# Kernel tuning notes

Hardware: AMD Instinct MI355X
Metric: run time of the kernel (lower is better)

## Reference

```python
import jax, jax.numpy as jnp
import numpy as np

B, T, C, H = 16, 2048, 1024, 128  # BATCH_SIZE, BLOCK_SIZE, EMBEDDING_SIZE, HEAD_SIZE


def setup_inputs() -> dict:
    key = jax.random.key(0)
    kx, kk, kq, kv = jax.random.split(key, 4)
    x = jax.random.normal(kx, (B, T, C), dtype=jnp.float32)
    # torch Linear(C, H, bias=False): y = x @ W^T with W [H, C]; we store W^T as [C, H]
    scale = C ** -0.5
    Wk = jax.random.normal(kk, (C, H), dtype=jnp.float32) * scale
    Wq = jax.random.normal(kq, (C, H), dtype=jnp.float32) * scale
    Wv = jax.random.normal(kv, (C, H), dtype=jnp.float32) * scale
    return {"x": x, "Wk": Wk, "Wq": Wq, "Wv": Wv}


def reference(x, Wk, Wq, Wv):
    # projections: [B, T, H]
    k = jnp.einsum("btc,ch->bth", x, Wk)
    q = jnp.einsum("btc,ch->bth", x, Wq)
    v = jnp.einsum("btc,ch->bth", x, Wv)
    # scaled scores: [B, T, T]
    scores = jnp.einsum("bqh,bkh->bqk", q, k) * (H ** -0.5)
    # causal mask (tril) then softmax over keys
    causal = jnp.tril(jnp.ones((T, T), dtype=bool))
    scores = jnp.where(causal, scores, -jnp.inf)
    weights = jax.nn.softmax(scores, axis=-1)
    # dropout with p=0.0 is identity (eval mode)
    return jnp.einsum("bqk,bkh->bqh", weights, v)
```

## Files before the change

### kernel.cpp

```cpp
#include <hip/hip_runtime.h>
#include <cmath>

#define B_ 16
#define T_ 2048
#define C_ 1024
#define H_ 128

#define BQ 64
#define BK 64
#define PS 68

#define PM 64
#define PK 64

typedef __bf16 bf16;
typedef bf16 bf16x8 __attribute__((ext_vector_type(8)));
typedef bf16 bf16x4 __attribute__((ext_vector_type(4)));
typedef float f32x4 __attribute__((ext_vector_type(4)));

#define GL_LDS16(gptr, lptr)                                                     \
    __builtin_amdgcn_global_load_lds(                                            \
        (const __attribute__((address_space(1))) unsigned int*)(gptr),           \
        (__attribute__((address_space(3))) unsigned int*)(lptr), 16, 0, 0)

__global__ __launch_bounds__(256) void convert_w(
    const float* __restrict__ Wq, const float* __restrict__ Wk,
    const float* __restrict__ Wv, bf16* __restrict__ wt)
{
    int gid = blockIdx.x * 256 + threadIdx.x;
    int w   = gid >> 14;
    int rem = gid & 16383;
    int n   = rem >> 7;
    int k0  = (rem & 127) * 8;
    const float* src = (w == 0) ? Wq : (w == 1) ? Wk : Wv;
    bf16x8 o;
#pragma unroll
    for (int j = 0; j < 8; ++j) o[j] = (bf16)src[(size_t)(k0 + j) * H_ + n];
    *(bf16x8*)(wt + (size_t)w * (H_ * C_) + (size_t)n * C_ + k0) = o;
}

__global__ __launch_bounds__(256, 2) void proj_mfma(
    const float* __restrict__ x, const bf16* __restrict__ wt,
    bf16* __restrict__ qb, bf16* __restrict__ kb, bf16* __restrict__ vtp)
{
    __shared__ bf16 xs[PM * PK];
    __shared__ bf16 ws[3 * H_ * PK];

    const int tid  = threadIdx.x;
    const int wave = tid >> 6;
    const int lane = tid & 63;
    const int quad = lane >> 4;
    const int lq   = lane & 15;
    const int wr   = wave >> 1;
    const int wc   = wave & 1;
    const int m0   = blockIdx.x * PM;

    f32x4 acc[3][2][4];
#pragma unroll
    for (int w = 0; w < 3; ++w)
#pragma unroll
        for (int mt = 0; mt < 2; ++mt)
#pragma unroll
            for (int nt = 0; nt < 4; ++nt)
                acc[w][mt][nt] = (f32x4){0.f, 0.f, 0.f, 0.f};

    int woff[12];
#pragma unroll
    for (int j = 0; j < 12; ++j) {
        int s  = (wave * 12 + j) * 64 + lane;
        int w  = s >> 10;
        int n  = (s >> 3) & 127;
        int cs = s & 7;
        int c  = cs ^ (n & 7);
        woff[j] = w * (H_ * C_) + n * C_ + c * 8;
    }
    int xoff[4], xslot[4];
#pragma unroll
    for (int j = 0; j < 4; ++j) {
        int f4  = j * 256 + tid;
        int row = f4 >> 4;
        int c4  = f4 & 15;
        int c   = c4 >> 1, half = c4 & 1;
        xoff[j]  = (m0 + row) * C_ + c4 * 4;
        xslot[j] = (row * 8 + (c ^ (row & 7))) * 8 + half * 4;
    }

    for (int k0 = 0; k0 < C_; k0 += PK) {
        __syncthreads();
#pragma unroll
        for (int j = 0; j < 12; ++j) {
            GL_LDS16(wt + woff[j] + k0, (char*)ws + (wave * 12 + j) * 1024);
        }
#pragma unroll
        for (int j = 0; j < 4; ++j) {
            float4 v = *(const float4*)(x + (size_t)xoff[j] + k0);
            bf16x4 o = {(bf16)v.x, (bf16)v.y, (bf16)v.z, (bf16)v.w};
            *(bf16x4*)&xs[xslot[j]] = o;
        }
        __syncthreads();

#pragma unroll
        for (int kc = 0; kc < 2; ++kc) {
            const int c = kc * 4 + quad;
            bf16x8 af[2];
#pragma unroll
            for (int mt = 0; mt < 2; ++mt) {
                int row  = wr * 32 + mt * 16 + lq;
                int slot = row * 8 + (c ^ (row & 7));
                af[mt] = *(const bf16x8*)&xs[slot * 8];
            }
#pragma unroll
            for (int w = 0; w < 3; ++w) {
#pragma unroll
                for (int nt = 0; nt < 4; ++nt) {
                    int n    = wc * 64 + nt * 16 + lq;
                    int slot = n * 8 + (c ^ (n & 7));
                    bf16x8 bfr = *(const bf16x8*)&ws[w * (H_ * PK) + slot * 8];
                    acc[w][0][nt] = __builtin_amdgcn_mfma_f32_16x16x32_bf16(af[0], bfr, acc[w][0][nt], 0, 0, 0);
                    acc[w][1][nt] = __builtin_amdgcn_mfma_f32_16x16x32_bf16(af[1], bfr, acc[w][1][nt], 0, 0, 0);
                }
            }
        }
    }

    const int b  = m0 >> 11;
    const int t0 = m0 & (T_ - 1);
#pragma unroll
    for (int w = 0; w < 2; ++w) {
        bf16* dst = (w == 0) ? qb : kb;
#pragma unroll
        for (int mt = 0; mt < 2; ++mt)
#pragma unroll
            for (int nt = 0; nt < 4; ++nt)
#pragma unroll
                for (int r = 0; r < 4; ++r) {
                    int row = m0 + wr * 32 + mt * 16 + quad * 4 + r;
                    int h   = wc * 64 + nt * 16 + lq;
                    dst[(size_t)row * H_ + h] = (bf16)acc[w][mt][nt][r];
                }
    }
#pragma unroll
    for (int mt = 0; mt < 2; ++mt)
#pragma unroll
        for (int nt = 0; nt < 4; ++nt) {
            int h = wc * 64 + nt * 16 + lq;
            int t = t0 + wr * 32 + mt * 16 + quad * 4;
            bf16x4 o = {(bf16)acc[2][mt][nt][0], (bf16)acc[2][mt][nt][1],
                        (bf16)acc[2][mt][nt][2], (bf16)acc[2][mt][nt][3]};
            *(bf16x4*)&vtp[((size_t)b * H_ + h) * T_ + t] = o;
        }
}

__global__ __launch_bounds__(256) void attn_mfma(
    const bf16* __restrict__ qb, const bf16* __restrict__ kb,
    const bf16* __restrict__ vt, float* __restrict__ out)
{
    __shared__ bf16 Ks[2][BK * 128];
    __shared__ bf16 Vs[2][128 * BK];
    __shared__ bf16 Ps[4][16 * PS];

    const int tid  = threadIdx.x;
    const int wave = tid >> 6;
    const int lane = tid & 63;
    const int quad = lane >> 4;
    const int lq   = lane & 15;

    const int bid = blockIdx.x;
    const int b   = bid & 15;
    const int jq  = bid >> 4;
    const int t0b = (31 - jq) * BQ;
    const int qt0 = t0b + wave * 16;

    const bf16* qrow = qb + ((size_t)b * T_ + qt0 + lq) * H_ + quad * 8;
    bf16x8 qf[4];
#pragma unroll
    for (int c = 0; c < 4; ++c) qf[c] = *(const bf16x8*)(qrow + 32 * c);

    f32x4 acc[8];
#pragma unroll
    for (int i = 0; i < 8; ++i) acc[i] = (f32x4){0.f, 0.f, 0.f, 0.f};
    f32x4 l_acc = (f32x4){0.f, 0.f, 0.f, 0.f};

    bf16x8 ones;
#pragma unroll
    for (int j = 0; j < 8; ++j) ones[j] = (bf16)1.0f;

    const float SC2 = 0.12751749985029928f;
    const int ntiles = t0b / BK + 1;

    const bf16* Kg = kb + (size_t)b * T_ * H_;
    const bf16* Vg = vt + (size_t)b * H_ * T_;
    bf16* Pw = &Ps[wave][0];

    int koff[4], voff[4], dst8[4];
#pragma unroll
    for (int j = 0; j < 4; ++j) {
        int p   = (j * 4 + wave) * 64 + lane;
        int r   = p >> 4, pos = p & 15;
        int l   = (pos & 8) | ((pos & 7) ^ (r & 7));
        koff[j] = r * H_ + l * 8;
        int hh  = p >> 3, pos2 = p & 7;
        voff[j] = hh * T_ + (pos2 ^ (hh & 7)) * 8;
        dst8[j] = (j * 4 + wave) * 64 * 8;
    }
    int swk[4], swv[2];
#pragma unroll
    for (int c = 0; c < 4; ++c) {
        int l = quad + 4 * c;
        swk[c] = (l & 8) | ((l & 7) ^ (lq & 7));
    }
#pragma unroll
    for (int kc = 0; kc < 2; ++kc) swv[kc] = (quad + 4 * kc) ^ (lq & 7);

#pragma unroll
    for (int j = 0; j < 4; ++j) {
        GL_LDS16(Kg + (size_t)koff[j], &Ks[0][dst8[j]]);
        GL_LDS16(Vg + (size_t)voff[j], &Vs[0][dst8[j]]);
    }

    for (int kt = 0; kt < ntiles; ++kt) {
        __syncthreads();
        if (kt + 1 < ntiles) {
            const int k1 = (kt + 1) * BK;
            const int nb = (kt + 1) & 1;
#pragma unroll
            for (int j = 0; j < 4; ++j) {
                GL_LDS16(Kg + (size_t)k1 * H_ + koff[j], &Ks[nb][dst8[j]]);
                GL_LDS16(Vg + (size_t)(k1 + voff[j]),    &Vs[nb][dst8[j]]);
            }
        }
        const bf16* Kb = &Ks[kt & 1][0];
        const bf16* Vb = &Vs[kt & 1][0];
        const bool finalt = (kt == ntiles - 1);

#pragma unroll
        for (int ns = 0; ns < 4; ++ns) {
            if (!finalt || ns <= wave) {
                f32x4 sv = (f32x4){0.f, 0.f, 0.f, 0.f};
#pragma unroll
                for (int c = 0; c < 4; ++c) {
                    bf16x8 kf = *(const bf16x8*)&Kb[((ns * 16 + lq) * 16 + swk[c]) * 8];
                    sv = __builtin_amdgcn_mfma_f32_16x16x32_bf16(qf[c], kf, sv, 0, 0, 0);
                }
                if (finalt && ns == wave) {
#pragma unroll
                    for (int r = 0; r < 4; ++r) {
                        float p = (lq <= quad * 4 + r) ? exp2f(sv[r] * SC2) : 0.f;
                        Pw[(quad * 4 + r) * PS + ns * 16 + lq] = (bf16)p;
                    }
                } else {
#pragma unroll
                    for (int r = 0; r < 4; ++r) {
                        Pw[(quad * 4 + r) * PS + ns * 16 + lq] = (bf16)exp2f(sv[r] * SC2);
                    }
                }
            } else {
#pragma unroll
                for (int r = 0; r < 4; ++r)
                    Pw[(quad * 4 + r) * PS + ns * 16 + lq] = (bf16)0.f;
            }
        }

        bf16x8 pf[2];
#pragma unroll
        for (int kc = 0; kc < 2; ++kc)
            pf[kc] = *(const bf16x8*)&Pw[lq * PS + kc * 32 + quad * 8];

        l_acc = __builtin_amdgcn_mfma_f32_16x16x32_bf16(pf[0], ones, l_acc, 0, 0, 0);
        l_acc = __builtin_amdgcn_mfma_f32_16x16x32_bf16(pf[1], ones, l_acc, 0, 0, 0);

#pragma unroll
        for (int ht = 0; ht < 8; ++ht) {
#pragma unroll
            for (int kc = 0; kc < 2; ++kc) {
                bf16x8 vf = *(const bf16x8*)&Vb[((ht * 16 + lq) * 8 + swv[kc]) * 8];
                acc[ht] = __builtin_amdgcn_mfma_f32_16x16x32_bf16(pf[kc], vf, acc[ht], 0, 0, 0);
            }
        }
    }

    float inv[4];
#pragma unroll
    for (int r = 0; r < 4; ++r) inv[r] = 1.f / l_acc[r];
#pragma unroll
    for (int ht = 0; ht < 8; ++ht) {
#pragma unroll
        for (int r = 0; r < 4; ++r) {
            out[((size_t)b * T_ + qt0 + quad * 4 + r) * H_ + ht * 16 + lq] = acc[ht][r] * inv[r];
        }
    }
}

extern "C" void kernel_launch(void* const* d_in, const int* in_sizes, int n_in,
                              void* d_out, int out_size, void* d_ws, size_t ws_size,
                              hipStream_t stream) {
    const float* x  = (const float*)d_in[0];
    const float* Wk = (const float*)d_in[1];
    const float* Wq = (const float*)d_in[2];
    const float* Wv = (const float*)d_in[3];
    float* out = (float*)d_out;

    bf16* qb = (bf16*)d_ws;
    bf16* kb = qb + (size_t)B_ * T_ * H_;
    bf16* vt = kb + (size_t)B_ * T_ * H_;
    bf16* wt = vt + (size_t)B_ * T_ * H_;

    convert_w<<<192, 256, 0, stream>>>(Wq, Wk, Wv, wt);

    proj_mfma<<<(B_ * T_) / PM, 256, 0, stream>>>(x, wt, qb, kb, vt);

    attn_mfma<<<(T_ / BQ) * B_, 256, 0, stream>>>(qb, kb, vt, out);
}
```

Measured before the change: 278.7 us.

## Restructure projection kernel: 512 threads, double-buffered weights, direct x register loads

The projection kernel now uses 128-row tiles with 512 threads (8 waves), so each block shares one weight tile across more rows. The weight slabs are double-buffered in LDS and the next slab is prefetched during compute, which removes one barrier per step. Activations are loaded straight from global memory into registers as MFMA fragments instead of being staged through LDS. Each block group starts at a different K phase to spread weight reads across memory. Strided per-lane global loads of x and a single block per CU with a larger LDS footprint may reduce latency hiding.

```diff
diff --git a/kernel.cpp b/kernel.cpp
--- a/kernel.cpp
+++ b/kernel.cpp
@@ -10,7 +10,7 @@
 #define BK 64
 #define PS 68
 
-#define PM 64
+#define PM 128
 #define PK 64
 
 typedef __bf16 bf16;
@@ -39,12 +39,11 @@
     *(bf16x8*)(wt + (size_t)w * (H_ * C_) + (size_t)n * C_ + k0) = o;
 }
 
-__global__ __launch_bounds__(256, 2) void proj_mfma(
+__global__ __launch_bounds__(512, 1) void proj_mfma(
     const float* __restrict__ x, const bf16* __restrict__ wt,
     bf16* __restrict__ qb, bf16* __restrict__ kb, bf16* __restrict__ vtp)
 {
-    __shared__ bf16 xs[PM * PK];
-    __shared__ bf16 ws[3 * H_ * PK];
+    __shared__ bf16 ws[2][3 * H_ * PK];
 
     const int tid  = threadIdx.x;
     const int wave = tid >> 6;
@@ -54,6 +53,7 @@
     const int wr   = wave >> 1;
     const int wc   = wave & 1;
     const int m0   = blockIdx.x * PM;
+    const int phase = (blockIdx.x >> 3) & 15;
 
     f32x4 acc[3][2][4];
 #pragma unroll
@@ -64,60 +64,63 @@
             for (int nt = 0; nt < 4; ++nt)
                 acc[w][mt][nt] = (f32x4){0.f, 0.f, 0.f, 0.f};
 
-    int woff[12];
-#pragma unroll
-    for (int j = 0; j < 12; ++j) {
-        int s  = (wave * 12 + j) * 64 + lane;
+    int woff[6];
+#pragma unroll
+    for (int j = 0; j < 6; ++j) {
+        int s  = (wave * 6 + j) * 64 + lane;
         int w  = s >> 10;
         int n  = (s >> 3) & 127;
         int cs = s & 7;
         int c  = cs ^ (n & 7);
         woff[j] = w * (H_ * C_) + n * C_ + c * 8;
     }
-    int xoff[4], xslot[4];
-#pragma unroll
-    for (int j = 0; j < 4; ++j) {
-        int f4  = j * 256 + tid;
-        int row = f4 >> 4;
-        int c4  = f4 & 15;
-        int c   = c4 >> 1, half = c4 & 1;
-        xoff[j]  = (m0 + row) * C_ + c4 * 4;
-        xslot[j] = (row * 8 + (c ^ (row & 7))) * 8 + half * 4;
-    }
-
-    for (int k0 = 0; k0 < C_; k0 += PK) {
+    int xbase[2];
+#pragma unroll
+    for (int mt = 0; mt < 2; ++mt)
+        xbase[mt] = (m0 + wr * 32 + mt * 16 + lq) * C_ + quad * 8;
+
+    {
+        const int k0 = phase * PK;
+#pragma unroll
+        for (int j = 0; j < 6; ++j)
+            GL_LDS16(wt + woff[j] + k0, (char*)ws[0] + (wave * 6 + j) * 1024);
+    }
+
+    const int NT = C_ / PK;
+    for (int t = 0; t < NT; ++t) {
+        const int cur = t & 1;
         __syncthreads();
-#pragma unroll
-        for (int j = 0; j < 12; ++j) {
-            GL_LDS16(wt + woff[j] + k0, (char*)ws + (wave * 12 + j) * 1024);
-        }
-#pragma unroll
-        for (int j = 0; j < 4; ++j) {
-            float4 v = *(const float4*)(x + (size_t)xoff[j] + k0);
-            bf16x4 o = {(bf16)v.x, (bf16)v.y, (bf16)v.z, (bf16)v.w};
-            *(bf16x4*)&xs[xslot[j]] = o;
-        }
-        __syncthreads();
+        if (t + 1 < NT) {
+            const int k1 = ((t + 1 + phase) & 15) * PK;
+#pragma unroll
+            for (int j = 0; j < 6; ++j)
+                GL_LDS16(wt + woff[j] + k1, (char*)ws[cur ^ 1] + (wave * 6 + j) * 1024);
+        }
+        const int kcur = ((t + phase) & 15) * PK;
+
+        bf16x8 af[2][2];
+#pragma unroll
+        for (int kc = 0; kc < 2; ++kc)
+#pragma unroll
+            for (int mt = 0; mt < 2; ++mt) {
+                float4 v0 = *(const float4*)(x + (size_t)xbase[mt] + kcur + kc * 32);
+                float4 v1 = *(const float4*)(x + (size_t)xbase[mt] + kcur + kc * 32 + 4);
+                af[kc][mt] = (bf16x8){(bf16)v0.x, (bf16)v0.y, (bf16)v0.z, (bf16)v0.w,
+                                      (bf16)v1.x, (bf16)v1.y, (bf16)v1.z, (bf16)v1.w};
+            }
 
 #pragma unroll
         for (int kc = 0; kc < 2; ++kc) {
             const int c = kc * 4 + quad;
-            bf16x8 af[2];
-#pragma unroll
-            for (int mt = 0; mt < 2; ++mt) {
-                int row  = wr * 32 + mt * 16 + lq;
-                int slot = row * 8 + (c ^ (row & 7));
-                af[mt] = *(const bf16x8*)&xs[slot * 8];
-            }
 #pragma unroll
             for (int w = 0; w < 3; ++w) {
 #pragma unroll
                 for (int nt = 0; nt < 4; ++nt) {
                     int n    = wc * 64 + nt * 16 + lq;
                     int slot = n * 8 + (c ^ (n & 7));
-                    bf16x8 bfr = *(const bf16x8*)&ws[w * (H_ * PK) + slot * 8];
-                    acc[w][0][nt] = __builtin_amdgcn_mfma_f32_16x16x32_bf16(af[0], bfr, acc[w][0][nt], 0, 0, 0);
-                    acc[w][1][nt] = __builtin_amdgcn_mfma_f32_16x16x32_bf16(af[1], bfr, acc[w][1][nt], 0, 0, 0);
+                    bf16x8 bfr = *(const bf16x8*)&ws[cur][w * (H_ * PK) + slot * 8];
+                    acc[w][0][nt] = __builtin_amdgcn_mfma_f32_16x16x32_bf16(af[kc][0], bfr, acc[w][0][nt], 0, 0, 0);
+                    acc[w][1][nt] = __builtin_amdgcn_mfma_f32_16x16x32_bf16(af[kc][1], bfr, acc[w][1][nt], 0, 0, 0);
                 }
             }
         }
@@ -144,10 +147,10 @@
 #pragma unroll
         for (int nt = 0; nt < 4; ++nt) {
             int h = wc * 64 + nt * 16 + lq;
-            int t = t0 + wr * 32 + mt * 16 + quad * 4;
+            int tt = t0 + wr * 32 + mt * 16 + quad * 4;
             bf16x4 o = {(bf16)acc[2][mt][nt][0], (bf16)acc[2][mt][nt][1],
                         (bf16)acc[2][mt][nt][2], (bf16)acc[2][mt][nt][3]};
-            *(bf16x4*)&vtp[((size_t)b * H_ + h) * T_ + t] = o;
+            *(bf16x4*)&vtp[((size_t)b * H_ + h) * T_ + tt] = o;
         }
 }
 
@@ -307,7 +310,7 @@
 
     convert_w<<<192, 256, 0, stream>>>(Wq, Wk, Wv, wt);
 
-    proj_mfma<<<(B_ * T_) / PM, 256, 0, stream>>>(x, wt, qb, kb, vt);
+    proj_mfma<<<(B_ * T_) / PM, 512, 0, stream>>>(x, wt, qb, kb, vt);
 
     attn_mfma<<<(T_ / BQ) * B_, 256, 0, stream>>>(qb, kb, vt, out);
 }
```

New measurement: 285.0 us. +2.3%, slower.
